# Kernel optimization log

Hardware: AMD Instinct MI355X
Metric: run time of the kernel (lower is better)

The kernel has to match this reference:

```python
import jax, jax.numpy as jnp
import numpy as np

B, N, CHANNELS = 4, 2048, 512
HEADS, HEAD_DIM = 8, 64
HIDDEN = HEADS * HEAD_DIM
ROPE_THETA = 10000.0


def _rotate_half(x):
    # interleaved pairs, as in rotary_embedding_torch
    x1 = x[..., 0::2]
    x2 = x[..., 1::2]
    return jnp.stack((-x2, x1), axis=-1).reshape(x.shape)


def _rope(x):
    # x: [b, h, n, d]; rotate over seq axis -2, full head dim
    n, d = x.shape[-2], x.shape[-1]
    inv_freq = 1.0 / (ROPE_THETA ** (jnp.arange(0, d, 2, dtype=jnp.float32) / d))
    freqs = jnp.arange(n, dtype=jnp.float32)[:, None] * inv_freq  # [n, d/2]
    freqs = jnp.repeat(freqs, 2, axis=-1)  # [n, d]
    return x * jnp.cos(freqs) + _rotate_half(x) * jnp.sin(freqs)


def setup_inputs() -> dict:
    key = jax.random.key(0)
    k1, k2, k3, k4 = jax.random.split(key, 4)
    x = jax.random.normal(k1, (B, N, CHANNELS), dtype=jnp.float32)
    pos_bias = jax.random.normal(k2, (HEADS, N, N), dtype=jnp.float32) * 0.02
    w_qkv = jax.random.normal(k3, (3 * HIDDEN, CHANNELS), dtype=jnp.float32) / np.sqrt(CHANNELS)
    w_out = jax.random.normal(k4, (CHANNELS, HIDDEN), dtype=jnp.float32) / np.sqrt(HIDDEN)
    return {"x": x, "pos_bias": pos_bias, "w_qkv": w_qkv, "w_out": w_out}


def reference(x, pos_bias, w_qkv, w_out):
    scale = HEAD_DIM ** -0.5
    b, n, _ = x.shape
    qkv = x @ w_qkv.T  # [b, n, 3*hidden]
    q, k, v = jnp.split(qkv, 3, axis=-1)

    def split_heads(z):
        return z.reshape(b, n, HEADS, HEAD_DIM).transpose(0, 2, 1, 3)  # [b,h,n,d]

    q, k, v = map(split_heads, (q, k, v))
    q = q * scale
    q = _rope(q)
    k = _rope(k)
    sim = jnp.einsum('bhid,bhjd->bhij', q, k) + pos_bias  # pos_bias [h,n,n] broadcasts
    attn = jax.nn.softmax(sim, axis=-1)  # matches sim - amax(detached) then softmax
    out = jnp.einsum('bhij,bhjd->bhid', attn, v)
    out = out.transpose(0, 2, 1, 3).reshape(b, n, HIDDEN)
    return out @ w_out.T
```

## Files before the change

### kernel.cpp

```cpp
#include <hip/hip_runtime.h>
#include <hip/hip_bf16.h>
#include <math.h>

typedef __bf16 bf16;
typedef bf16  bf16x8 __attribute__((ext_vector_type(8)));
typedef bf16  bf16x4 __attribute__((ext_vector_type(4)));
typedef float f32x4  __attribute__((ext_vector_type(4)));
typedef float f32x16 __attribute__((ext_vector_type(16)));
typedef unsigned int u32x2 __attribute__((ext_vector_type(2)));
typedef unsigned int u32x4 __attribute__((ext_vector_type(4)));

#define B_   4
#define N_   2048
#define CH_  512
#define H_   8
#define D_   64
#define HID_ 512

__device__ __forceinline__ f32x4 mfma16(bf16x8 a, bf16x8 b, f32x4 c) {
    return __builtin_amdgcn_mfma_f32_16x16x32_bf16(a, b, c, 0, 0, 0);
}
__device__ __forceinline__ f32x16 mfma32(bf16x8 a, bf16x8 b, f32x16 c) {
    return __builtin_amdgcn_mfma_f32_32x32x16_bf16(a, b, c, 0, 0, 0);
}

__global__ void rope_table_k(float* __restrict__ cosT, float* __restrict__ sinT) {
    int idx = blockIdx.x * 256 + threadIdx.x;
    int pos = idx >> 5, fi = idx & 31;
    double inv = pow(10000.0, -(double)(2 * fi) / 64.0);
    double ang = (double)pos * inv;
    cosT[idx] = (float)cos(ang);
    sinT[idx] = (float)sin(ang);
}

__global__ __launch_bounds__(256) void qkv_rope_k(
    const float* __restrict__ x, const float* __restrict__ w,
    const float* __restrict__ cosT, const float* __restrict__ sinT,
    bf16* __restrict__ Qb, bf16* __restrict__ Kb, bf16* __restrict__ Vt)
{
    __shared__ __align__(16) bf16 Xs[128][40];
    __shared__ __align__(16) bf16 Ws[128][40];
    const int tid = threadIdx.x, lane = tid & 63, wid = tid >> 6;
    const int wr = wid >> 1, wc = wid & 1;
    const int m0 = blockIdx.x * 128, n0 = blockIdx.y * 128;
    const int l15 = lane & 15, l4 = lane >> 4;
    const int sr = tid >> 1, sh = (tid & 1) * 16;

    f32x4 acc[4][4] = {};

    for (int kt = 0; kt < 16; ++kt) {
        __syncthreads();
        {
            const float4* xp = reinterpret_cast<const float4*>(x + (size_t)(m0 + sr) * CH_ + kt * 32 + sh);
            const float4* wp = reinterpret_cast<const float4*>(w + (size_t)(n0 + sr) * CH_ + kt * 32 + sh);
#pragma unroll
            for (int j = 0; j < 4; ++j) {
                float4 f = xp[j];
                bf16x4 o1 = { (bf16)f.x, (bf16)f.y, (bf16)f.z, (bf16)f.w };
                *reinterpret_cast<bf16x4*>(&Xs[sr][sh + j * 4]) = o1;
                float4 g = wp[j];
                bf16x4 o2 = { (bf16)g.x, (bf16)g.y, (bf16)g.z, (bf16)g.w };
                *reinterpret_cast<bf16x4*>(&Ws[sr][sh + j * 4]) = o2;
            }
        }
        __syncthreads();
        bf16x8 a[4], bb[4];
#pragma unroll
        for (int mf = 0; mf < 4; ++mf)
            a[mf] = *reinterpret_cast<const bf16x8*>(&Xs[wr * 64 + mf * 16 + l15][l4 * 8]);
#pragma unroll
        for (int nf = 0; nf < 4; ++nf)
            bb[nf] = *reinterpret_cast<const bf16x8*>(&Ws[wc * 64 + nf * 16 + l15][l4 * 8]);
#pragma unroll
        for (int mf = 0; mf < 4; ++mf)
#pragma unroll
            for (int nf = 0; nf < 4; ++nf)
                acc[mf][nf] = mfma16(a[mf], bb[nf], acc[mf][nf]);
    }

#pragma unroll
    for (int nf = 0; nf < 4; ++nf) {
        const int col = n0 + wc * 64 + nf * 16 + l15;
        const int sec = col >> 9;
        const int cc = col & 511;
        const int hh = cc >> 6, dd = cc & 63;
        if (sec == 2) {
#pragma unroll
            for (int mf = 0; mf < 4; ++mf) {
                const int pos0 = m0 + wr * 64 + mf * 16 + l4 * 4;
                const int bb_ = pos0 >> 11, pos = pos0 & 2047;
                bf16x4 pk = { (bf16)acc[mf][nf][0], (bf16)acc[mf][nf][1],
                              (bf16)acc[mf][nf][2], (bf16)acc[mf][nf][3] };
                *reinterpret_cast<bf16x4*>(
                    Vt + ((size_t)(bb_ * H_ + hh) * D_ + dd) * N_ + pos) = pk;
            }
        } else {
            const float sgn = (dd & 1) ? 1.f : -1.f;
#pragma unroll
            for (int mf = 0; mf < 4; ++mf) {
#pragma unroll
                for (int i = 0; i < 4; ++i) {
                    const int row = m0 + wr * 64 + mf * 16 + l4 * 4 + i;
                    const int bb_ = row >> 11, pos = row & 2047;
                    const float v = acc[mf][nf][i];
                    const float v2 = __shfl_xor(v, 1);
                    const size_t dst = ((size_t)((bb_ * H_ + hh) * N_ + pos)) * D_ + dd;
                    const float c = cosT[pos * 32 + (dd >> 1)];
                    const float s = sinT[pos * 32 + (dd >> 1)];
                    const float r = v * c + sgn * v2 * s;
                    if (sec == 0) Qb[dst] = (bf16)(r * 0.125f);
                    else          Kb[dst] = (bf16)r;
                }
            }
        }
    }
}

#define KRD2(kt2,kc) (((kt2)*32 + l31)*128 + (((kc)*32 + l5*16) ^ (l7<<4)))
#define VRD2(dt,kt)  (((dt)*32 + l31)*128 + (((kt)*32 + l5*16) ^ (l7<<4)))

__global__ __launch_bounds__(128, 2) void attn_k(
    const bf16* __restrict__ Qb, const bf16* __restrict__ Kb, const bf16* __restrict__ Vt,
    const float* __restrict__ bias, bf16* __restrict__ AO)
{
    __shared__ __align__(16) unsigned char KsB[2][8192];
    __shared__ __align__(16) unsigned char VsB[2][8192];

    const int tid = threadIdx.x, lane = tid & 63, wid = tid >> 6;
    const int l31 = lane & 31, l5 = lane >> 5, l7 = lane & 7;
    const int id = blockIdx.x;
    const int xcd = id & 7, j = id >> 3;
    const int bh = xcd + 8 * (j >> 5);
    const int qt = j & 31;
    const int b = bh >> 3, h = bh & 7;
    const int q0 = qt * 64 + wid * 32;
    const size_t bhoff = (size_t)bh * N_ * D_;

    bf16x8 qreg[4];
#pragma unroll
    for (int kc = 0; kc < 4; ++kc)
        qreg[kc] = *reinterpret_cast<const bf16x8*>(
            Qb + bhoff + (size_t)(q0 + l31) * D_ + kc * 16 + l5 * 8);

    const unsigned scol = ((lane & 7) * 16) ^ ((lane >> 3) << 4);
    const char* kg = (const char*)(Kb + bhoff) + (size_t)(wid * 32 + (lane >> 3)) * 128 + scol;
    const char* vg = (const char*)(Vt + bhoff) + (size_t)(wid * 32 + (lane >> 3)) * (N_ * 2) + scol;

    const float* bp = bias + ((size_t)h * N_ + (q0 + l31)) * N_ + l5 * 4;

#define GLL(src, dst) __builtin_amdgcn_global_load_lds( \
        (const __attribute__((address_space(1))) unsigned int*)(src), \
        (__attribute__((address_space(3))) unsigned int*)(dst), 16, 0, 0)

#define STAGE(buf, t) do { \
        GLL(kg + (size_t)(t) * 8192,            &KsB[buf][wid * 4096]); \
        GLL(kg + (size_t)(t) * 8192 + 1024,     &KsB[buf][wid * 4096 + 1024]); \
        GLL(kg + (size_t)(t) * 8192 + 2048,     &KsB[buf][wid * 4096 + 2048]); \
        GLL(kg + (size_t)(t) * 8192 + 3072,     &KsB[buf][wid * 4096 + 3072]); \
        GLL(vg + (size_t)(t) * 128,             &VsB[buf][wid * 4096]); \
        GLL(vg + (size_t)(t) * 128 + 32768,     &VsB[buf][wid * 4096 + 1024]); \
        GLL(vg + (size_t)(t) * 128 + 65536,     &VsB[buf][wid * 4096 + 2048]); \
        GLL(vg + (size_t)(t) * 128 + 98304,     &VsB[buf][wid * 4096 + 3072]); \
    } while (0)

#define PIPE_SYNC() do { \
        asm volatile("s_waitcnt vmcnt(8)" ::: "memory"); \
        __builtin_amdgcn_sched_barrier(0); \
        __builtin_amdgcn_s_barrier(); \
        __builtin_amdgcn_sched_barrier(0); \
    } while (0)

    f32x16 o[2] = {};
    float lp = 0.f;
    f32x4 bc[2][4], bn[2][4], b2[2][4];

    STAGE(0, 0);
    __builtin_amdgcn_sched_barrier(0);
#pragma unroll
    for (int kt2 = 0; kt2 < 2; ++kt2)
#pragma unroll
        for (int r2 = 0; r2 < 4; ++r2) {
            bc[kt2][r2] = *reinterpret_cast<const f32x4*>(bp + kt2 * 32 + r2 * 8);
            bn[kt2][r2] = *reinterpret_cast<const f32x4*>(bp + 64 + kt2 * 32 + r2 * 8);
        }
    PIPE_SYNC();

#pragma unroll 2
    for (int kb = 0; kb < 32; ++kb) {
        const int cur = kb & 1;
        if (kb < 31) {
            STAGE(cur ^ 1, kb + 1);
            __builtin_amdgcn_sched_barrier(0);
        }
        if (kb < 30) {
#pragma unroll
            for (int kt2 = 0; kt2 < 2; ++kt2)
#pragma unroll
                for (int r2 = 0; r2 < 4; ++r2)
                    b2[kt2][r2] = *reinterpret_cast<const f32x4*>(
                        bp + (size_t)(kb + 2) * 64 + kt2 * 32 + r2 * 8);
        }

        const unsigned char* ksC = &KsB[cur][0];
        f32x16 s[2] = {};
        __builtin_amdgcn_s_setprio(1);
#pragma unroll
        for (int kt2 = 0; kt2 < 2; ++kt2) {
#pragma unroll
            for (int kc = 0; kc < 4; ++kc) {
                bf16x8 kf = *reinterpret_cast<const bf16x8*>(ksC + KRD2(kt2, kc));
                s[kt2] = mfma32(kf, qreg[kc], s[kt2]);
            }
        }
        __builtin_amdgcn_s_setprio(0);

        bf16x8 pa[4];
#pragma unroll
        for (int kt2 = 0; kt2 < 2; ++kt2) {
            unsigned U[4][2], R[4][2];
#pragma unroll
            for (int r2 = 0; r2 < 4; ++r2) {
                float p0 = __expf(s[kt2][r2 * 4 + 0] + bc[kt2][r2][0]);
                float p1 = __expf(s[kt2][r2 * 4 + 1] + bc[kt2][r2][1]);
                float p2 = __expf(s[kt2][r2 * 4 + 2] + bc[kt2][r2][2]);
                float p3 = __expf(s[kt2][r2 * 4 + 3] + bc[kt2][r2][3]);
                lp += (p0 + p1) + (p2 + p3);
                bf16x4 pk = { (bf16)p0, (bf16)p1, (bf16)p2, (bf16)p3 };
                u32x2 uu = __builtin_bit_cast(u32x2, pk);
                U[r2][0] = uu[0];
                U[r2][1] = uu[1];
            }
#pragma unroll
            for (int r2 = 0; r2 < 4; ++r2) {
                R[r2][0] = __shfl_xor(U[r2][0], 32);
                R[r2][1] = __shfl_xor(U[r2][1], 32);
            }
            const bool hi = (l5 != 0);
#pragma unroll
            for (int ktp = 0; ktp < 2; ++ktp) {
                unsigned g0 = hi ? R[2 * ktp + 1][0] : U[2 * ktp][0];
                unsigned g1 = hi ? R[2 * ktp + 1][1] : U[2 * ktp][1];
                unsigned h0 = hi ? U[2 * ktp + 1][0] : R[2 * ktp][0];
                unsigned h1 = hi ? U[2 * ktp + 1][1] : R[2 * ktp][1];
                u32x4 wv = { g0, g1, h0, h1 };
                pa[kt2 * 2 + ktp] = __builtin_bit_cast(bf16x8, wv);
            }
        }

        const unsigned char* vsC = &VsB[cur][0];
        __builtin_amdgcn_s_setprio(1);
#pragma unroll
        for (int kt = 0; kt < 4; ++kt) {
#pragma unroll
            for (int dt = 0; dt < 2; ++dt) {
                bf16x8 vf = *reinterpret_cast<const bf16x8*>(vsC + VRD2(dt, kt));
                o[dt] = mfma32(pa[kt], vf, o[dt]);
            }
        }
        __builtin_amdgcn_s_setprio(0);

#pragma unroll
        for (int kt2 = 0; kt2 < 2; ++kt2)
#pragma unroll
            for (int r2 = 0; r2 < 4; ++r2) {
                bc[kt2][r2] = bn[kt2][r2];
                bn[kt2][r2] = b2[kt2][r2];
            }

        PIPE_SYNC();
    }

    float tot = lp;
    tot += __shfl_xor(tot, 32);
    float rv[16];
#pragma unroll
    for (int reg = 0; reg < 16; ++reg) {
        const int qr = (reg & 3) + 8 * (reg >> 2) + 4 * l5;
        rv[reg] = 1.0f / __shfl(tot, qr);
    }
#pragma unroll
    for (int dt = 0; dt < 2; ++dt)
#pragma unroll
        for (int reg = 0; reg < 16; ++reg) {
            const int qr = (reg & 3) + 8 * (reg >> 2) + 4 * l5;
            AO[((size_t)(b * N_ + q0 + qr)) * HID_ + h * D_ + dt * 32 + l31] =
                (bf16)(o[dt][reg] * rv[reg]);
        }
}

__global__ __launch_bounds__(256) void proj_k(
    const bf16* __restrict__ A, const float* __restrict__ w, float* __restrict__ out)
{
    __shared__ __align__(16) bf16 As[128][40];
    __shared__ __align__(16) bf16 Ws[128][40];
    const int tid = threadIdx.x, lane = tid & 63, wid = tid >> 6;
    const int wr = wid >> 1, wc = wid & 1;
    const int m0 = blockIdx.x * 128, n0 = blockIdx.y * 128;
    const int l15 = lane & 15, l4 = lane >> 4;
    const int sr = tid >> 1, sh = (tid & 1) * 16;

    f32x4 acc[4][4] = {};

    for (int kt = 0; kt < 16; ++kt) {
        __syncthreads();
        {
            const bf16* ap = A + (size_t)(m0 + sr) * HID_ + kt * 32 + sh;
            *reinterpret_cast<bf16x8*>(&As[sr][sh])     = *reinterpret_cast<const bf16x8*>(ap);
            *reinterpret_cast<bf16x8*>(&As[sr][sh + 8]) = *reinterpret_cast<const bf16x8*>(ap + 8);
            const float4* wp = reinterpret_cast<const float4*>(w + (size_t)(n0 + sr) * HID_ + kt * 32 + sh);
#pragma unroll
            for (int j = 0; j < 4; ++j) {
                float4 g = wp[j];
                bf16x4 o2 = { (bf16)g.x, (bf16)g.y, (bf16)g.z, (bf16)g.w };
                *reinterpret_cast<bf16x4*>(&Ws[sr][sh + j * 4]) = o2;
            }
        }
        __syncthreads();
        bf16x8 a[4], bb[4];
#pragma unroll
        for (int mf = 0; mf < 4; ++mf)
            a[mf] = *reinterpret_cast<const bf16x8*>(&As[wr * 64 + mf * 16 + l15][l4 * 8]);
#pragma unroll
        for (int nf = 0; nf < 4; ++nf)
            bb[nf] = *reinterpret_cast<const bf16x8*>(&Ws[wc * 64 + nf * 16 + l15][l4 * 8]);
#pragma unroll
        for (int mf = 0; mf < 4; ++mf)
#pragma unroll
            for (int nf = 0; nf < 4; ++nf)
                acc[mf][nf] = mfma16(a[mf], bb[nf], acc[mf][nf]);
    }
#pragma unroll
    for (int nf = 0; nf < 4; ++nf) {
        const int col = n0 + wc * 64 + nf * 16 + l15;
#pragma unroll
        for (int mf = 0; mf < 4; ++mf) {
#pragma unroll
            for (int i = 0; i < 4; ++i) {
                const int row = m0 + wr * 64 + mf * 16 + l4 * 4 + i;
                out[(size_t)row * HID_ + col] = acc[mf][nf][i];
            }
        }
    }
}

extern "C" void kernel_launch(void* const* d_in, const int* in_sizes, int n_in,
                              void* d_out, int out_size, void* d_ws, size_t ws_size,
                              hipStream_t stream) {
    (void)in_sizes; (void)n_in; (void)out_size; (void)ws_size;
    const float* x     = (const float*)d_in[0];
    const float* bias  = (const float*)d_in[1];
    const float* w_qkv = (const float*)d_in[2];
    const float* w_out = (const float*)d_in[3];
    float* out = (float*)d_out;

    bf16* Qb = (bf16*)d_ws;
    bf16* Kb = Qb + 4194304;
    bf16* Vt = Kb + 4194304;
    bf16* AO = Vt + 4194304;
    float* cosT = (float*)(AO + 4194304);
    float* sinT = cosT + 65536;

    rope_table_k<<<dim3(256), 256, 0, stream>>>(cosT, sinT);
    qkv_rope_k  <<<dim3(64, 12), 256, 0, stream>>>(x, w_qkv, cosT, sinT, Qb, Kb, Vt);
    attn_k      <<<dim3(1024), 128, 0, stream>>>(Qb, Kb, Vt, bias, AO);
    proj_k      <<<dim3(64, 4), 256, 0, stream>>>(AO, w_out, out);
}
```

Measured before the change: 156.4 us.

## Split attention into single-wave blocks with private K/V staging and no barriers

The attention kernel now uses one 64-thread wave per block, each handling 32 query rows. It streams 32-key K/V tiles into its own LDS double buffer and runs twice the grid size. The workgroup s_barrier is dropped: each wave synchronises only on its own vmcnt, with a tighter count so the bias prefetch loads can stay in flight. The aim is to remove barrier stalls and let more independent waves hide the memory-bound bias stream. The cost is that each wave now loads K/V itself instead of sharing them across two waves, and each loop iteration does half as much MFMA work, so fixed per-iteration overhead counts for more.

```diff
diff --git a/kernel.cpp b/kernel.cpp
--- a/kernel.cpp
+++ b/kernel.cpp
@@ -116,24 +116,24 @@
     }
 }
 
-#define KRD2(kt2,kc) (((kt2)*32 + l31)*128 + (((kc)*32 + l5*16) ^ (l7<<4)))
-#define VRD2(dt,kt)  (((dt)*32 + l31)*128 + (((kt)*32 + l5*16) ^ (l7<<4)))
-
-__global__ __launch_bounds__(128, 2) void attn_k(
+#define KRD32(kc)    (l31*128 + (((kc)*32 + l5*16) ^ ((l31&7)<<4)))
+#define VRD32(dt,kt) (l31*128 + (((dt)*64 + (kt)*32 + l5*16) ^ ((l31&7)<<4)))
+
+__global__ __launch_bounds__(64, 4) void attn_k(
     const bf16* __restrict__ Qb, const bf16* __restrict__ Kb, const bf16* __restrict__ Vt,
     const float* __restrict__ bias, bf16* __restrict__ AO)
 {
-    __shared__ __align__(16) unsigned char KsB[2][8192];
-    __shared__ __align__(16) unsigned char VsB[2][8192];
-
-    const int tid = threadIdx.x, lane = tid & 63, wid = tid >> 6;
-    const int l31 = lane & 31, l5 = lane >> 5, l7 = lane & 7;
+    __shared__ __align__(16) unsigned char KsB[2][4096];
+    __shared__ __align__(16) unsigned char VsB[2][4096];
+
+    const int lane = threadIdx.x & 63;
+    const int l31 = lane & 31, l5 = lane >> 5;
     const int id = blockIdx.x;
     const int xcd = id & 7, j = id >> 3;
-    const int bh = xcd + 8 * (j >> 5);
-    const int qt = j & 31;
+    const int bh = xcd + 8 * (j >> 6);
+    const int qt = j & 63;
     const int b = bh >> 3, h = bh & 7;
-    const int q0 = qt * 64 + wid * 32;
+    const int q0 = qt * 32;
     const size_t bhoff = (size_t)bh * N_ * D_;
 
     bf16x8 qreg[4];
@@ -142,9 +142,10 @@
         qreg[kc] = *reinterpret_cast<const bf16x8*>(
             Qb + bhoff + (size_t)(q0 + l31) * D_ + kc * 16 + l5 * 8);
 
-    const unsigned scol = ((lane & 7) * 16) ^ ((lane >> 3) << 4);
-    const char* kg = (const char*)(Kb + bhoff) + (size_t)(wid * 32 + (lane >> 3)) * 128 + scol;
-    const char* vg = (const char*)(Vt + bhoff) + (size_t)(wid * 32 + (lane >> 3)) * (N_ * 2) + scol;
+    const unsigned kcol = ((lane & 7) * 16) ^ ((lane >> 3) << 4);
+    const char* kg = (const char*)(Kb + bhoff) + (size_t)(lane >> 3) * 128 + kcol;
+    const char* vg = (const char*)(Vt + bhoff)
+        + (size_t)((lane >> 3) + 32 * (kcol >> 6)) * (N_ * 2) + (kcol & 63);
 
     const float* bp = bias + ((size_t)h * N_ + (q0 + l31)) * N_ + l5 * 4;
 
@@ -153,77 +154,67 @@
         (__attribute__((address_space(3))) unsigned int*)(dst), 16, 0, 0)
 
 #define STAGE(buf, t) do { \
-        GLL(kg + (size_t)(t) * 8192,            &KsB[buf][wid * 4096]); \
-        GLL(kg + (size_t)(t) * 8192 + 1024,     &KsB[buf][wid * 4096 + 1024]); \
-        GLL(kg + (size_t)(t) * 8192 + 2048,     &KsB[buf][wid * 4096 + 2048]); \
-        GLL(kg + (size_t)(t) * 8192 + 3072,     &KsB[buf][wid * 4096 + 3072]); \
-        GLL(vg + (size_t)(t) * 128,             &VsB[buf][wid * 4096]); \
-        GLL(vg + (size_t)(t) * 128 + 32768,     &VsB[buf][wid * 4096 + 1024]); \
-        GLL(vg + (size_t)(t) * 128 + 65536,     &VsB[buf][wid * 4096 + 2048]); \
-        GLL(vg + (size_t)(t) * 128 + 98304,     &VsB[buf][wid * 4096 + 3072]); \
+        GLL(kg + (size_t)(t) * 4096,            &KsB[buf][0]); \
+        GLL(kg + (size_t)(t) * 4096 + 1024,     &KsB[buf][1024]); \
+        GLL(kg + (size_t)(t) * 4096 + 2048,     &KsB[buf][2048]); \
+        GLL(kg + (size_t)(t) * 4096 + 3072,     &KsB[buf][3072]); \
+        GLL(vg + (size_t)(t) * 64,              &VsB[buf][0]); \
+        GLL(vg + (size_t)(t) * 64 + 8 * N_ * 2,  &VsB[buf][1024]); \
+        GLL(vg + (size_t)(t) * 64 + 16 * N_ * 2, &VsB[buf][2048]); \
+        GLL(vg + (size_t)(t) * 64 + 24 * N_ * 2, &VsB[buf][3072]); \
     } while (0)
 
-#define PIPE_SYNC() do { \
-        asm volatile("s_waitcnt vmcnt(8)" ::: "memory"); \
-        __builtin_amdgcn_sched_barrier(0); \
-        __builtin_amdgcn_s_barrier(); \
+#define WAITN(n) do { \
+        asm volatile("s_waitcnt vmcnt(" #n ")" ::: "memory"); \
         __builtin_amdgcn_sched_barrier(0); \
     } while (0)
 
     f32x16 o[2] = {};
     float lp = 0.f;
-    f32x4 bc[2][4], bn[2][4], b2[2][4];
+    f32x4 bc[4], bn[4], b2[4];
 
     STAGE(0, 0);
     __builtin_amdgcn_sched_barrier(0);
 #pragma unroll
-    for (int kt2 = 0; kt2 < 2; ++kt2)
-#pragma unroll
-        for (int r2 = 0; r2 < 4; ++r2) {
-            bc[kt2][r2] = *reinterpret_cast<const f32x4*>(bp + kt2 * 32 + r2 * 8);
-            bn[kt2][r2] = *reinterpret_cast<const f32x4*>(bp + 64 + kt2 * 32 + r2 * 8);
-        }
-    PIPE_SYNC();
+    for (int r2 = 0; r2 < 4; ++r2) {
+        bc[r2] = *reinterpret_cast<const f32x4*>(bp + r2 * 8);
+        bn[r2] = *reinterpret_cast<const f32x4*>(bp + 32 + r2 * 8);
+    }
+    WAITN(8);
 
 #pragma unroll 2
-    for (int kb = 0; kb < 32; ++kb) {
+    for (int kb = 0; kb < 64; ++kb) {
         const int cur = kb & 1;
-        if (kb < 31) {
+        if (kb < 63) {
             STAGE(cur ^ 1, kb + 1);
             __builtin_amdgcn_sched_barrier(0);
         }
-        if (kb < 30) {
-#pragma unroll
-            for (int kt2 = 0; kt2 < 2; ++kt2)
-#pragma unroll
-                for (int r2 = 0; r2 < 4; ++r2)
-                    b2[kt2][r2] = *reinterpret_cast<const f32x4*>(
-                        bp + (size_t)(kb + 2) * 64 + kt2 * 32 + r2 * 8);
+        if (kb < 62) {
+#pragma unroll
+            for (int r2 = 0; r2 < 4; ++r2)
+                b2[r2] = *reinterpret_cast<const f32x4*>(
+                    bp + (size_t)(kb + 2) * 32 + r2 * 8);
         }
 
         const unsigned char* ksC = &KsB[cur][0];
-        f32x16 s[2] = {};
+        f32x16 s = {};
         __builtin_amdgcn_s_setprio(1);
 #pragma unroll
-        for (int kt2 = 0; kt2 < 2; ++kt2) {
-#pragma unroll
-            for (int kc = 0; kc < 4; ++kc) {
-                bf16x8 kf = *reinterpret_cast<const bf16x8*>(ksC + KRD2(kt2, kc));
-                s[kt2] = mfma32(kf, qreg[kc], s[kt2]);
-            }
+        for (int kc = 0; kc < 4; ++kc) {
+            bf16x8 kf = *reinterpret_cast<const bf16x8*>(ksC + KRD32(kc));
+            s = mfma32(kf, qreg[kc], s);
         }
         __builtin_amdgcn_s_setprio(0);
 
-        bf16x8 pa[4];
-#pragma unroll
-        for (int kt2 = 0; kt2 < 2; ++kt2) {
+        bf16x8 pa[2];
+        {
             unsigned U[4][2], R[4][2];
 #pragma unroll
             for (int r2 = 0; r2 < 4; ++r2) {
-                float p0 = __expf(s[kt2][r2 * 4 + 0] + bc[kt2][r2][0]);
-                float p1 = __expf(s[kt2][r2 * 4 + 1] + bc[kt2][r2][1]);
-                float p2 = __expf(s[kt2][r2 * 4 + 2] + bc[kt2][r2][2]);
-                float p3 = __expf(s[kt2][r2 * 4 + 3] + bc[kt2][r2][3]);
+                float p0 = __expf(s[r2 * 4 + 0] + bc[r2][0]);
+                float p1 = __expf(s[r2 * 4 + 1] + bc[r2][1]);
+                float p2 = __expf(s[r2 * 4 + 2] + bc[r2][2]);
+                float p3 = __expf(s[r2 * 4 + 3] + bc[r2][3]);
                 lp += (p0 + p1) + (p2 + p3);
                 bf16x4 pk = { (bf16)p0, (bf16)p1, (bf16)p2, (bf16)p3 };
                 u32x2 uu = __builtin_bit_cast(u32x2, pk);
@@ -243,31 +234,29 @@
                 unsigned h0 = hi ? U[2 * ktp + 1][0] : R[2 * ktp][0];
                 unsigned h1 = hi ? U[2 * ktp + 1][1] : R[2 * ktp][1];
                 u32x4 wv = { g0, g1, h0, h1 };
-                pa[kt2 * 2 + ktp] = __builtin_bit_cast(bf16x8, wv);
+                pa[ktp] = __builtin_bit_cast(bf16x8, wv);
             }
         }
 
         const unsigned char* vsC = &VsB[cur][0];
         __builtin_amdgcn_s_setprio(1);
 #pragma unroll
-        for (int kt = 0; kt < 4; ++kt) {
+        for (int kt = 0; kt < 2; ++kt) {
 #pragma unroll
             for (int dt = 0; dt < 2; ++dt) {
-                bf16x8 vf = *reinterpret_cast<const bf16x8*>(vsC + VRD2(dt, kt));
+                bf16x8 vf = *reinterpret_cast<const bf16x8*>(vsC + VRD32(dt, kt));
                 o[dt] = mfma32(pa[kt], vf, o[dt]);
             }
         }
         __builtin_amdgcn_s_setprio(0);
 
 #pragma unroll
-        for (int kt2 = 0; kt2 < 2; ++kt2)
-#pragma unroll
-            for (int r2 = 0; r2 < 4; ++r2) {
-                bc[kt2][r2] = bn[kt2][r2];
-                bn[kt2][r2] = b2[kt2][r2];
-            }
-
-        PIPE_SYNC();
+        for (int r2 = 0; r2 < 4; ++r2) {
+            bc[r2] = bn[r2];
+            bn[r2] = b2[r2];
+        }
+
+        if (kb < 62) { WAITN(4); } else { WAITN(0); }
     }
 
     float tot = lp;
@@ -362,6 +351,6 @@
 
     rope_table_k<<<dim3(256), 256, 0, stream>>>(cosT, sinT);
     qkv_rope_k  <<<dim3(64, 12), 256, 0, stream>>>(x, w_qkv, cosT, sinT, Qb, Kb, Vt);
-    attn_k      <<<dim3(1024), 128, 0, stream>>>(Qb, Kb, Vt, bias, AO);
+    attn_k      <<<dim3(2048), 64, 0, stream>>>(Qb, Kb, Vt, bias, AO);
     proj_k      <<<dim3(64, 4), 256, 0, stream>>>(AO, w_out, out);
 }
```

After: 179.2 us. +14.6%, slower.
